# Performance work log

Hardware: AMD Instinct MI355X
Metric: run time of the kernel (lower is better)

## Reference

```python
import jax, jax.numpy as jnp
from jax import lax
import numpy as np

W_DIM = 512
B, CIN, COUT, H = 16, 128, 128, 128
KS = 3
UP, DOWN = 2, 2
TAPS = 12
GAIN = float(np.sqrt(2.0))
SLOPE = 0.2
CLAMP = 256.0
# gauss_spline(0, n=1) = 1/sqrt(2*pi*(n+1)/12); zero_filter = sqrt(f*f) = f at alpha=1
ZF = float(1.0 / np.sqrt(2.0 * np.pi / 6.0))


def _lowpass(numtaps, cutoff, fs, beta=8.0):
    # Kaiser-windowed sinc lowpass, normalized to unit DC gain (stands in for design_lowpass_filter)
    n = np.arange(numtaps) - (numtaps - 1) / 2.0
    h = np.sinc(2.0 * cutoff / fs * n) * np.kaiser(numtaps, beta)
    return jnp.asarray((h / h.sum()).astype(np.float32))


def setup_inputs() -> dict:
    key = jax.random.key(0)
    ks = jax.random.split(key, 6)
    fs_tmp = 128 * UP  # tmp_sampling_rate = max(in_sr,out_sr)*lrelu_upsampling
    return {
        "x": jax.random.normal(ks[0], (B, CIN, H, H), jnp.float32),
        "w": jax.random.normal(ks[1], (B, W_DIM), jnp.float32),
        "affine_weight": jax.random.normal(ks[2], (CIN, W_DIM), jnp.float32),
        "affine_bias": jnp.ones((CIN,), jnp.float32),  # bias_init=1
        "kernel_weight": jax.random.normal(ks[3], (COUT, CIN, KS, KS), jnp.float32),
        "bias": jnp.zeros((COUT,), jnp.float32),
        "up_filter": _lowpass(TAPS, 64.0, fs_tmp),
        "down_filter": _lowpass(TAPS, 64.0, fs_tmp),
        "magnitude_ema": jnp.ones((), jnp.float32),
    }


def reference(x, w, affine_weight, affine_bias, kernel_weight, bias, up_filter, down_filter, magnitude_ema):
    # --- affine (FullyConnectedLayer, linear): weight_gain = 1/sqrt(in_features) ---
    s = w @ (affine_weight.T * (1.0 / np.sqrt(W_DIM))) + affine_bias  # [B, CIN]

    # --- SynthesisGroupKernel: kernel = test_weight * zero_filter * gain(ks); gain=1, zf const ---
    wk = kernel_weight * ZF  # [COUT, CIN, 3, 3]

    # --- modulated_conv2d (demodulate=True) ---
    wk = wk * lax.rsqrt(jnp.mean(wk * wk, axis=(1, 2, 3), keepdims=True))
    s = s * lax.rsqrt(jnp.mean(s * s))
    ww = wk[None] * s[:, None, :, None, None]                      # [B, COUT, CIN, 3, 3]
    dcoefs = lax.rsqrt(jnp.sum(ww * ww, axis=(2, 3, 4)) + 1e-8)    # [B, COUT]
    ww = ww * dcoefs[:, :, None, None, None]
    ww = ww * (magnitude_ema ** -0.5)                              # input_gain = ema.rsqrt()
    xg = x.reshape(1, B * CIN, H, H)
    wg = ww.reshape(B * COUT, CIN, KS, KS)
    y = lax.conv_general_dilated(xg, wg, (1, 1), [(1, 1), (1, 1)], feature_group_count=B)
    y = y.reshape(B, COUT, H, H)

    # --- filtered_lrelu: FIR upsample x2, bias + lrelu + gain + clamp, FIR downsample x2 ---
    fu2 = jnp.outer(up_filter, up_filter) * (UP * UP)              # up gain folded into filter
    fd2 = jnp.outer(down_filter, down_filter)
    wu = jnp.broadcast_to(fu2, (COUT, 1, TAPS, TAPS))
    wd = jnp.broadcast_to(fd2, (COUT, 1, TAPS, TAPS))
    # upsample: zero-stuff via lhs_dilation; 128 -> 256
    y = lax.conv_general_dilated(y, wu, (1, 1), [(6, 6), (6, 6)], lhs_dilation=(UP, UP),
                                 feature_group_count=COUT)
    y = y + bias[None, :, None, None]
    y = jnp.where(y >= 0, y, y * SLOPE) * GAIN
    y = jnp.clip(y, -CLAMP, CLAMP)
    # downsample: FIR + stride 2; 256 -> 128
    y = lax.conv_general_dilated(y, wd, (DOWN, DOWN), [(5, 5), (5, 5)], feature_group_count=COUT)
    return y
```

## Files before the change

kernel.cpp:

```cpp
#include <hip/hip_runtime.h>

typedef unsigned short ushort_t;
typedef __attribute__((ext_vector_type(8))) short bf16x8;
typedef __attribute__((ext_vector_type(4))) float f32x4;
typedef __attribute__((ext_vector_type(4))) unsigned int u32x4;

#define ZF 0.9770840884556017f
#define SQ2 1.4142135623730951f

__device__ __forceinline__ ushort_t f2bf(float f) {
    unsigned u = __float_as_uint(f);
    unsigned r = (u + 0x7fffu + ((u >> 16) & 1u)) >> 16;
    return (ushort_t)r;
}
__device__ __forceinline__ float bf2f(ushort_t h) {
    return __uint_as_float(((unsigned)h) << 16);
}

__global__ void kzero(float* ssum) { if (threadIdx.x == 0) ssum[0] = 0.f; }

__global__ __launch_bounds__(128) void ks(const float* __restrict__ w,
                                          const float* __restrict__ aw,
                                          const float* __restrict__ ab,
                                          float* sbuf, float* ssum) {
    int b = blockIdx.x, c = threadIdx.x;
    const float4* wp = (const float4*)(w + b * 512);
    const float4* ap = (const float4*)(aw + c * 512);
    float acc = 0.f;
    for (int k = 0; k < 128; ++k) {
        float4 xv = wp[k], yv = ap[k];
        acc += xv.x * yv.x + xv.y * yv.y + xv.z * yv.z + xv.w * yv.w;
    }
    float s = acc * 0.04419417382415922f + ab[c];
    sbuf[b * 128 + c] = s;
    float sq = s * s;
#pragma unroll
    for (int m = 1; m < 64; m <<= 1) sq += __shfl_xor(sq, m);
    if ((c & 63) == 0) atomicAdd(ssum, sq);
}

__global__ __launch_bounds__(128) void kkn(const float* __restrict__ kw,
                                           const float* __restrict__ ssum,
                                           float* kn, float* srstd) {
    int o = blockIdx.x, t = threadIdx.x;
    float acc = 0.f;
    for (int j = t; j < 1152; j += 128) { float v = kw[o * 1152 + j] * ZF; acc += v * v; }
#pragma unroll
    for (int m = 1; m < 64; m <<= 1) acc += __shfl_xor(acc, m);
    __shared__ float red[2];
    if ((t & 63) == 0) red[t >> 6] = acc;
    __syncthreads();
    if (t == 0) {
        kn[o] = ZF * rsqrtf((red[0] + red[1]) * (1.0f / 1152.0f));
        if (o == 0) srstd[0] = rsqrtf(ssum[0] * (1.0f / 2048.0f));
    }
}

__global__ __launch_bounds__(128) void kww(const float* __restrict__ kw,
                                           const float* __restrict__ sbuf,
                                           const float* __restrict__ kn,
                                           const float* __restrict__ srstd,
                                           const float* __restrict__ ema,
                                           ushort_t* __restrict__ wwbf) {
    int o = blockIdx.x, b = blockIdx.y, i = threadIdx.x;
    float sn = sbuf[b * 128 + i] * srstd[0];
    float knv = kn[o];
    const float* kwp = kw + (o * 128 + i) * 9;
    float wv[9];
    float ssq = 0.f;
#pragma unroll
    for (int t = 0; t < 9; ++t) { float v = kwp[t] * knv * sn; wv[t] = v; ssq += v * v; }
#pragma unroll
    for (int m = 1; m < 64; m <<= 1) ssq += __shfl_xor(ssq, m);
    __shared__ float red[2];
    if ((i & 63) == 0) red[i >> 6] = ssq;
    __syncthreads();
    float tot = red[0] + red[1];
    float g = rsqrtf(tot + 1e-8f) * rsqrtf(ema[0]);
#pragma unroll
    for (int t = 0; t < 9; ++t)
        wwbf[((size_t)(b * 128 + o)) * 1152 + t * 128 + i] = f2bf(wv[t] * g);
}

__global__ __launch_bounds__(256) void kT(const float* __restrict__ x, ushort_t* __restrict__ xT) {
    int h = blockIdx.x, b = blockIdx.y;
    __shared__ ushort_t tile[128 * 132];
    int tid = threadIdx.x;
    const float* xb = x + (size_t)b * 2097152 + (size_t)h * 128;
#pragma unroll 4
    for (int it = 0; it < 16; ++it) {
        int idx = it * 256 + tid;
        int cin = idx >> 5, c4 = idx & 31;
        float4 v = *(const float4*)(xb + (size_t)cin * 16384 + c4 * 4);
        union { ushort_t us[4]; unsigned long long u; } p;
        p.us[0] = f2bf(v.x); p.us[1] = f2bf(v.y); p.us[2] = f2bf(v.z); p.us[3] = f2bf(v.w);
        *(unsigned long long*)(tile + cin * 132 + c4 * 4) = p.u;
    }
    __syncthreads();
    ushort_t* ob = xT + ((size_t)(b * 128 + h)) * 16384;
#pragma unroll 2
    for (int it = 0; it < 8; ++it) {
        int idx = it * 256 + tid;
        int wcol = idx >> 4;
        int cinb = (idx & 15) << 3;
        union { ushort_t us[8]; u32x4 v; } p;
#pragma unroll
        for (int j = 0; j < 8; ++j) p.us[j] = tile[(cinb + j) * 132 + wcol];
        *(u32x4*)(ob + (size_t)wcol * 128 + cinb) = p.v;
    }
}

__global__ __launch_bounds__(256) void kC(const ushort_t* __restrict__ xT,
                                          const ushort_t* __restrict__ wwbf,
                                          ushort_t* __restrict__ ybf) {
    const int b = blockIdx.y;
    const int tile = blockIdx.x;
    const int R0 = (tile >> 3) * 8;
    const int C0 = (tile & 7) * 16;
    const int tid = threadIdx.x;
    const int wid = tid >> 6;
    const int lane = tid & 63;
    const int lr = lane & 15;
    const int lg = lane >> 4;

    __shared__ __align__(16) unsigned char xs[10 * 18 * 128 * 2];

    const ushort_t* xTb = xT + (size_t)b * 2097152;
    for (int q = tid; q < 2880; q += 256) {
        int cinb = (q & 15) << 3;
        int rc = q >> 4;
        int row = rc / 18;
        int col = rc - row * 18;
        int gr = R0 - 1 + row, gc = C0 - 1 + col;
        u32x4 v = {0u, 0u, 0u, 0u};
        if ((unsigned)gr < 128u && (unsigned)gc < 128u)
            v = *(const u32x4*)(xTb + (((size_t)(gr << 7) + gc) << 7) + cinb);
        int byte = (rc << 8) + (cinb << 1);
        byte ^= (col & 7) << 4;
        *(u32x4*)(xs + byte) = v;
    }
    __syncthreads();

    const ushort_t* wwp = wwbf + ((size_t)(b * 128 + wid * 32)) * 1152;
    f32x4 acc[2][8] = {};
#pragma unroll 1
    for (int tap = 0; tap < 9; ++tap) {
        const int dr = tap / 3, dc = tap - dr * 3;
#pragma unroll
        for (int kq = 0; kq < 4; ++kq) {
            const int kloc = kq * 32 + lg * 8;
            const int kglob = tap * 128 + kloc;
            bf16x8 a0 = *(const bf16x8*)(wwp + lr * 1152 + kglob);
            bf16x8 a1 = *(const bf16x8*)(wwp + (lr + 16) * 1152 + kglob);
#pragma unroll
            for (int nf = 0; nf < 8; ++nf) {
                int col = lr + dc;
                int byte = (((nf + dr) * 18 + col) << 8) + (kloc << 1);
                byte ^= (col & 7) << 4;
                bf16x8 bfr = *(const bf16x8*)(xs + byte);
                acc[0][nf] = __builtin_amdgcn_mfma_f32_16x16x32_bf16(a0, bfr, acc[0][nf], 0, 0, 0);
                acc[1][nf] = __builtin_amdgcn_mfma_f32_16x16x32_bf16(a1, bfr, acc[1][nf], 0, 0, 0);
            }
        }
    }

    ushort_t* yb = ybf + (size_t)b * 2097152;
#pragma unroll
    for (int mf = 0; mf < 2; ++mf)
#pragma unroll
        for (int nf = 0; nf < 8; ++nf)
#pragma unroll
            for (int r = 0; r < 4; ++r) {
                int cout = wid * 32 + mf * 16 + lg * 4 + r;
                int row = R0 + nf, colp = C0 + lr;
                yb[(((size_t)cout << 7) + row) * 128 + colp] = f2bf(acc[mf][nf][r]);
            }
}

__global__ __launch_bounds__(256) void kF(const ushort_t* __restrict__ ybf,
                                          const float* __restrict__ bias,
                                          const float* __restrict__ upf,
                                          const float* __restrict__ dnf,
                                          float* __restrict__ out) {
    int tileid = blockIdx.x, co = blockIdx.y, b = blockIdx.z;
    int R0 = (tileid >> 2) * 32, C0 = (tileid & 3) * 32;
    int tid = threadIdx.x;
    __shared__ float A[74 * 77];
    __shared__ float Bm[42 * 76];

    float fue[6], fuo[6], fre[6], fro[6], fd[12];
#pragma unroll
    for (int m = 0; m < 6; ++m) {
        float e = 2.0f * upf[2 * m], o = 2.0f * upf[2 * m + 1];
        fue[m] = e; fuo[m] = o;
        fre[m] = SQ2 * e; fro[m] = SQ2 * o;
    }
#pragma unroll
    for (int j = 0; j < 12; ++j) fd[j] = dnf[j];
    float bv = SQ2 * bias[co];

    const ushort_t* ych = ybf + ((size_t)(b * 128 + co) << 14);
    int yr0 = R0 - 5, yc0 = C0 - 5;
    for (int idx = tid; idx < 1764; idx += 256) {
        int r = idx / 42, c = idx - r * 42;
        int gr = yr0 + r, gc = yc0 + c;
        float v = 0.f;
        if ((unsigned)gr < 128u && (unsigned)gc < 128u) v = bf2f(ych[(gr << 7) + gc]);
        A[r * 44 + c] = v;
    }
    __syncthreads();
    for (int it = tid; it < 42 * 37; it += 256) {
        int r = it / 37, k = it - r * 37;
        const float* yr = A + r * 44 + k;
        float y0 = yr[0], y1 = yr[1], y2 = yr[2], y3 = yr[3], y4 = yr[4], y5 = yr[5];
        float s0 = fuo[0] * y0 + fuo[1] * y1 + fuo[2] * y2 + fuo[3] * y3 + fuo[4] * y4 + fuo[5] * y5;
        float s1 = fue[0] * y0 + fue[1] * y1 + fue[2] * y2 + fue[3] * y3 + fue[4] * y4 + fue[5] * y5;
        float2 sv; sv.x = s0; sv.y = s1;
        *(float2*)(Bm + r * 76 + 2 * k) = sv;
    }
    __syncthreads();
    for (int it = tid; it < 37 * 37; it += 256) {
        int kr = it / 37, jc = it - kr * 37;
        const float* bc = Bm + kr * 76 + 2 * jc;
        float2 c0 = *(const float2*)(bc);
        float2 c1 = *(const float2*)(bc + 76);
        float2 c2 = *(const float2*)(bc + 152);
        float2 c3 = *(const float2*)(bc + 228);
        float2 c4 = *(const float2*)(bc + 304);
        float2 c5 = *(const float2*)(bc + 380);
        float t00 = bv + fro[0] * c0.x + fro[1] * c1.x + fro[2] * c2.x + fro[3] * c3.x + fro[4] * c4.x + fro[5] * c5.x;
        float t01 = bv + fro[0] * c0.y + fro[1] * c1.y + fro[2] * c2.y + fro[3] * c3.y + fro[4] * c4.y + fro[5] * c5.y;
        float t10 = bv + fre[0] * c0.x + fre[1] * c1.x + fre[2] * c2.x + fre[3] * c3.x + fre[4] * c4.x + fre[5] * c5.x;
        float t11 = bv + fre[0] * c0.y + fre[1] * c1.y + fre[2] * c2.y + fre[3] * c3.y + fre[4] * c4.y + fre[5] * c5.y;
        t00 = fmaxf(t00, 0.f) + 0.2f * fminf(t00, 0.f);
        t01 = fmaxf(t01, 0.f) + 0.2f * fminf(t01, 0.f);
        t10 = fmaxf(t10, 0.f) + 0.2f * fminf(t10, 0.f);
        t11 = fmaxf(t11, 0.f) + 0.2f * fminf(t11, 0.f);
        t00 = fminf(fmaxf(t00, -256.f), 256.f);
        t01 = fminf(fmaxf(t01, -256.f), 256.f);
        t10 = fminf(fmaxf(t10, -256.f), 256.f);
        t11 = fminf(fmaxf(t11, -256.f), 256.f);
        float* zp = A + (2 * kr) * 77 + 2 * jc;
        zp[0] = t00; zp[1] = t01;
        zp[77] = t10; zp[78] = t11;
    }
    __syncthreads();
    {
        bool tz = (R0 == 0), bz = (R0 == 96), lz = (C0 == 0), rz = (C0 == 96);
        if (tz || bz) {
            for (int idx = tid; idx < 370; idx += 256) {
                int s = idx / 74, c = idx - s * 74;
                if (tz) A[s * 77 + c] = 0.f;
                if (bz) A[(69 + s) * 77 + c] = 0.f;
            }
        }
        if (lz || rz) {
            for (int idx = tid; idx < 370; idx += 256) {
                int r = idx / 5, s = idx - r * 5;
                if (lz) A[r * 77 + s] = 0.f;
                if (rz) A[r * 77 + 69 + s] = 0.f;
            }
        }
        if (tz || bz || lz || rz) __syncthreads();
    }
    for (int it = tid; it < 74 * 8; it += 256) {
        int ur = it >> 3, q = it & 7;
        const float* z = A + ur * 77 + 8 * q;
        float win[18];
#pragma unroll
        for (int j = 0; j < 18; ++j) win[j] = z[j];
        float* dp = Bm + ur * 33 + 4 * q;
#pragma unroll
        for (int i = 0; i < 4; ++i) {
            float s = 0.f;
#pragma unroll
            for (int j = 0; j < 12; ++j) s += fd[j] * win[2 * i + j];
            dp[i] = s;
        }
    }
    __syncthreads();
    {
        int qr = tid >> 5, oc = tid & 31;
        const float* d = Bm + (8 * qr) * 33 + oc;
        float win[18];
#pragma unroll
        for (int j = 0; j < 18; ++j) win[j] = d[j * 33];
        float* ob = out + (((size_t)(b * 128 + co) << 7) + R0) * 128 + C0 + oc;
#pragma unroll
        for (int i = 0; i < 4; ++i) {
            float s = 0.f;
#pragma unroll
            for (int j = 0; j < 12; ++j) s += fd[j] * win[2 * i + j];
            ob[(4 * qr + i) * 128] = s;
        }
    }
}

extern "C" void kernel_launch(void* const* d_in, const int* in_sizes, int n_in,
                              void* d_out, int out_size, void* d_ws, size_t ws_size,
                              hipStream_t stream) {
    const float* x    = (const float*)d_in[0];
    const float* w    = (const float*)d_in[1];
    const float* aw   = (const float*)d_in[2];
    const float* ab   = (const float*)d_in[3];
    const float* kw   = (const float*)d_in[4];
    const float* bias = (const float*)d_in[5];
    const float* upf  = (const float*)d_in[6];
    const float* dnf  = (const float*)d_in[7];
    const float* ema  = (const float*)d_in[8];
    float* out = (float*)d_out;
    char* ws = (char*)d_ws;

    float* sbuf  = (float*)ws;
    float* ssum  = (float*)(ws + 8192);
    float* srstd = (float*)(ws + 8196);
    float* kn    = (float*)(ws + 8448);
    ushort_t* wwbf = (ushort_t*)(ws + 16384);
    ushort_t* xT   = (ushort_t*)(ws + ((size_t)5 << 20));
    ushort_t* ybf  = (ushort_t*)(ws + ((size_t)5 << 20) + ((size_t)64 << 20));

    kzero<<<1, 64, 0, stream>>>(ssum);
    ks<<<16, 128, 0, stream>>>(w, aw, ab, sbuf, ssum);
    kkn<<<128, 128, 0, stream>>>(kw, ssum, kn, srstd);
    kww<<<dim3(128, 16), 128, 0, stream>>>(kw, sbuf, kn, srstd, ema, wwbf);
    kT<<<dim3(128, 16), 256, 0, stream>>>(x, xT);
    kC<<<dim3(128, 16), 256, 0, stream>>>(xT, wwbf, ybf);
    kF<<<dim3(16, 128, 16), 256, 0, stream>>>(ybf, bias, upf, dnf, out);
}
```

Measured before the change: 597.9 us.

## Pre-swizzle modulated weights into MFMA fragment layout and pack FIR math into float2

The demodulation kernel now writes bf16 weights in a tap/k-quarter/lane-group-major layout. This lets each conv wave load its A fragments as contiguous 16-byte vectors that coalesce across lanes, replacing strided row reads. The filtered-lrelu kernel rewrites the upsample, bias/lrelu/clamp and both downsample passes with 2-wide float vectors so the compiler can emit packed FMA instructions. It also simplifies leaky-relu to max(x, 0.2x) and remaps the final-pass threads to store float2 outputs. The risks are extra register pressure from the wider windows and the different thread-to-output mapping in the last pass.

```diff
diff --git a/kernel.cpp b/kernel.cpp
--- a/kernel.cpp
+++ b/kernel.cpp
@@ -3,6 +3,7 @@
 typedef unsigned short ushort_t;
 typedef __attribute__((ext_vector_type(8))) short bf16x8;
 typedef __attribute__((ext_vector_type(4))) float f32x4;
+typedef __attribute__((ext_vector_type(2))) float f32x2;
 typedef __attribute__((ext_vector_type(4))) unsigned int u32x4;
 
 #define ZF 0.9770840884556017f
@@ -77,9 +78,11 @@
     __syncthreads();
     float tot = red[0] + red[1];
     float g = rsqrtf(tot + 1e-8f) * rsqrtf(ema[0]);
+    int kq = i >> 5, lg = (i >> 3) & 3, j = i & 7;
+    size_t base = (size_t)b * 147456 + (size_t)kq * 4096 + (size_t)lg * 1024 + (size_t)o * 8 + j;
 #pragma unroll
     for (int t = 0; t < 9; ++t)
-        wwbf[((size_t)(b * 128 + o)) * 1152 + t * 128 + i] = f2bf(wv[t] * g);
+        wwbf[base + (size_t)t * 16384] = f2bf(wv[t] * g);
 }
 
 __global__ __launch_bounds__(256) void kT(const float* __restrict__ x, ushort_t* __restrict__ xT) {
@@ -141,17 +144,17 @@
     }
     __syncthreads();
 
-    const ushort_t* wwp = wwbf + ((size_t)(b * 128 + wid * 32)) * 1152;
+    const ushort_t* wwp = wwbf + (size_t)b * 147456 + (size_t)lg * 1024 + (size_t)(wid * 32 + lr) * 8;
     f32x4 acc[2][8] = {};
 #pragma unroll 1
     for (int tap = 0; tap < 9; ++tap) {
         const int dr = tap / 3, dc = tap - dr * 3;
 #pragma unroll
         for (int kq = 0; kq < 4; ++kq) {
+            const ushort_t* wb = wwp + (size_t)tap * 16384 + (size_t)kq * 4096;
+            bf16x8 a0 = *(const bf16x8*)(wb);
+            bf16x8 a1 = *(const bf16x8*)(wb + 128);
             const int kloc = kq * 32 + lg * 8;
-            const int kglob = tap * 128 + kloc;
-            bf16x8 a0 = *(const bf16x8*)(wwp + lr * 1152 + kglob);
-            bf16x8 a1 = *(const bf16x8*)(wwp + (lr + 16) * 1152 + kglob);
 #pragma unroll
             for (int nf = 0; nf < 8; ++nf) {
                 int col = lr + dc;
@@ -188,12 +191,13 @@
     __shared__ float A[74 * 77];
     __shared__ float Bm[42 * 76];
 
-    float fue[6], fuo[6], fre[6], fro[6], fd[12];
+    f32x2 fuv[6];
+    float fro[6], fre[6], fd[12];
 #pragma unroll
     for (int m = 0; m < 6; ++m) {
         float e = 2.0f * upf[2 * m], o = 2.0f * upf[2 * m + 1];
-        fue[m] = e; fuo[m] = o;
-        fre[m] = SQ2 * e; fro[m] = SQ2 * o;
+        fuv[m].x = o; fuv[m].y = e;
+        fro[m] = SQ2 * o; fre[m] = SQ2 * e;
     }
 #pragma unroll
     for (int j = 0; j < 12; ++j) fd[j] = dnf[j];
@@ -212,34 +216,33 @@
     for (int it = tid; it < 42 * 37; it += 256) {
         int r = it / 37, k = it - r * 37;
         const float* yr = A + r * 44 + k;
-        float y0 = yr[0], y1 = yr[1], y2 = yr[2], y3 = yr[3], y4 = yr[4], y5 = yr[5];
-        float s0 = fuo[0] * y0 + fuo[1] * y1 + fuo[2] * y2 + fuo[3] * y3 + fuo[4] * y4 + fuo[5] * y5;
-        float s1 = fue[0] * y0 + fue[1] * y1 + fue[2] * y2 + fue[3] * y3 + fue[4] * y4 + fue[5] * y5;
-        float2 sv; sv.x = s0; sv.y = s1;
-        *(float2*)(Bm + r * 76 + 2 * k) = sv;
+        f32x2 sv = {0.f, 0.f};
+#pragma unroll
+        for (int m = 0; m < 6; ++m) {
+            float ym = yr[m];
+            f32x2 yv = {ym, ym};
+            sv = fuv[m] * yv + sv;
+        }
+        *(f32x2*)(Bm + r * 76 + 2 * k) = sv;
     }
     __syncthreads();
     for (int it = tid; it < 37 * 37; it += 256) {
         int kr = it / 37, jc = it - kr * 37;
         const float* bc = Bm + kr * 76 + 2 * jc;
-        float2 c0 = *(const float2*)(bc);
-        float2 c1 = *(const float2*)(bc + 76);
-        float2 c2 = *(const float2*)(bc + 152);
-        float2 c3 = *(const float2*)(bc + 228);
-        float2 c4 = *(const float2*)(bc + 304);
-        float2 c5 = *(const float2*)(bc + 380);
-        float t00 = bv + fro[0] * c0.x + fro[1] * c1.x + fro[2] * c2.x + fro[3] * c3.x + fro[4] * c4.x + fro[5] * c5.x;
-        float t01 = bv + fro[0] * c0.y + fro[1] * c1.y + fro[2] * c2.y + fro[3] * c3.y + fro[4] * c4.y + fro[5] * c5.y;
-        float t10 = bv + fre[0] * c0.x + fre[1] * c1.x + fre[2] * c2.x + fre[3] * c3.x + fre[4] * c4.x + fre[5] * c5.x;
-        float t11 = bv + fre[0] * c0.y + fre[1] * c1.y + fre[2] * c2.y + fre[3] * c3.y + fre[4] * c4.y + fre[5] * c5.y;
-        t00 = fmaxf(t00, 0.f) + 0.2f * fminf(t00, 0.f);
-        t01 = fmaxf(t01, 0.f) + 0.2f * fminf(t01, 0.f);
-        t10 = fmaxf(t10, 0.f) + 0.2f * fminf(t10, 0.f);
-        t11 = fmaxf(t11, 0.f) + 0.2f * fminf(t11, 0.f);
-        t00 = fminf(fmaxf(t00, -256.f), 256.f);
-        t01 = fminf(fmaxf(t01, -256.f), 256.f);
-        t10 = fminf(fmaxf(t10, -256.f), 256.f);
-        t11 = fminf(fmaxf(t11, -256.f), 256.f);
+        f32x2 bv2 = {bv, bv};
+        f32x2 tv0 = bv2, tv1 = bv2;
+#pragma unroll
+        for (int m = 0; m < 6; ++m) {
+            f32x2 cm = *(const f32x2*)(bc + 76 * m);
+            f32x2 fo = {fro[m], fro[m]};
+            f32x2 fe = {fre[m], fre[m]};
+            tv0 = fo * cm + tv0;
+            tv1 = fe * cm + tv1;
+        }
+        float t00 = fminf(fmaxf(fmaxf(tv0.x, 0.2f * tv0.x), -256.f), 256.f);
+        float t01 = fminf(fmaxf(fmaxf(tv0.y, 0.2f * tv0.y), -256.f), 256.f);
+        float t10 = fminf(fmaxf(fmaxf(tv1.x, 0.2f * tv1.x), -256.f), 256.f);
+        float t11 = fminf(fmaxf(fmaxf(tv1.y, 0.2f * tv1.y), -256.f), 256.f);
         float* zp = A + (2 * kr) * 77 + 2 * jc;
         zp[0] = t00; zp[1] = t01;
         zp[77] = t10; zp[78] = t11;
@@ -263,35 +266,45 @@
         }
         if (tz || bz || lz || rz) __syncthreads();
     }
-    for (int it = tid; it < 74 * 8; it += 256) {
-        int ur = it >> 3, q = it & 7;
-        const float* z = A + ur * 77 + 8 * q;
-        float win[18];
-#pragma unroll
-        for (int j = 0; j < 18; ++j) win[j] = z[j];
-        float* dp = Bm + ur * 33 + 4 * q;
+    for (int it = tid; it < 296; it += 256) {
+        int urp = it >> 3, q = it & 7;
+        const float* z0 = A + (2 * urp) * 77 + 8 * q;
+        const float* z1 = z0 + 77;
+        f32x2 w2[18];
+#pragma unroll
+        for (int j = 0; j < 18; ++j) { w2[j].x = z0[j]; w2[j].y = z1[j]; }
+        float* dp = Bm + (2 * urp) * 33 + 4 * q;
 #pragma unroll
         for (int i = 0; i < 4; ++i) {
-            float s = 0.f;
-#pragma unroll
-            for (int j = 0; j < 12; ++j) s += fd[j] * win[2 * i + j];
-            dp[i] = s;
+            f32x2 s = {0.f, 0.f};
+#pragma unroll
+            for (int j = 0; j < 12; ++j) {
+                f32x2 fv = {fd[j], fd[j]};
+                s = fv * w2[2 * i + j] + s;
+            }
+            dp[i] = s.x; dp[33 + i] = s.y;
         }
     }
     __syncthreads();
     {
-        int qr = tid >> 5, oc = tid & 31;
-        const float* d = Bm + (8 * qr) * 33 + oc;
-        float win[18];
-#pragma unroll
-        for (int j = 0; j < 18; ++j) win[j] = d[j * 33];
-        float* ob = out + (((size_t)(b * 128 + co) << 7) + R0) * 128 + C0 + oc;
-#pragma unroll
-        for (int i = 0; i < 4; ++i) {
-            float s = 0.f;
-#pragma unroll
-            for (int j = 0; j < 12; ++j) s += fd[j] * win[2 * i + j];
-            ob[(4 * qr + i) * 128] = s;
+        int u = tid & 15, g = tid >> 4;
+        const float* dbase = Bm + 2 * u;
+        f32x2 w2[14];
+#pragma unroll
+        for (int j = 0; j < 14; ++j) {
+            const float* p = dbase + (4 * g + j) * 33;
+            w2[j].x = p[0]; w2[j].y = p[1];
+        }
+        float* ob = out + (((size_t)(b * 128 + co) << 7) + R0 + 2 * g) * 128 + C0 + 2 * u;
+#pragma unroll
+        for (int i = 0; i < 2; ++i) {
+            f32x2 s = {0.f, 0.f};
+#pragma unroll
+            for (int j = 0; j < 12; ++j) {
+                f32x2 fv = {fd[j], fd[j]};
+                s = fv * w2[2 * i + j] + s;
+            }
+            *(f32x2*)(ob + i * 128) = s;
         }
     }
 }
```

Measured after the change: 603.9 us. No clear change (+1.0%).
